# Optimization experiments

Hardware: AMD Instinct MI355X
Metric: run time of the kernel (lower is better)

## Reference

```python
import jax, jax.numpy as jnp
import numpy as np

N_NODES = 50000
N_EDGES = 640000
D = 128  # node_dim == edge_dim (required by gate * Vh[dst])
BN_EPS = 1e-5


def _bn(x, gamma, beta):
    # BatchNorm1d in training mode: batch stats over dim 0, biased variance.
    mu = jnp.mean(x, axis=0)
    var = jnp.var(x, axis=0)
    return (x - mu) * jax.lax.rsqrt(var + BN_EPS) * gamma + beta


def setup_inputs() -> dict:
    key = jax.random.key(0)
    ks = jax.random.split(key, 12)
    s = 1.0 / np.sqrt(D)
    h = jax.random.normal(ks[0], (N_NODES, D), dtype=jnp.float32)
    e = jax.random.normal(ks[1], (N_EDGES, D), dtype=jnp.float32)
    edge_index = jax.random.randint(ks[2], (2, N_EDGES), 0, N_NODES)
    mk = lambda k: jax.random.uniform(k, (D, D), jnp.float32, -s, s)
    return {
        "h": h, "e": e, "edge_index": edge_index,
        "Pw": mk(ks[3]), "Qw": mk(ks[4]), "Rw": mk(ks[5]),
        "Uw": mk(ks[6]), "Vw": mk(ks[7]),
        "W1": mk(ks[8]), "b1": jnp.zeros((D,), jnp.float32),
        "W2": mk(ks[9]), "b2": jnp.zeros((D,), jnp.float32),
        "gamma_e": jnp.ones((D,), jnp.float32), "beta_e": jnp.zeros((D,), jnp.float32),
        "gamma_n": jnp.ones((D,), jnp.float32), "beta_n": jnp.zeros((D,), jnp.float32),
        "alpha": jnp.float32(1.0),
    }


def reference(h, e, edge_index, Pw, Qw, Rw, Uw, Vw, W1, b1, W2, b2,
              gamma_e, beta_e, gamma_n, beta_n, alpha):
    src, dst = edge_index[0], edge_index[1]
    # e_hat = P e + Q h[src] + R h[dst]   -> [E, D]
    e_hat = e @ Pw + h[src] @ Qw + h[dst] @ Rw
    # edge update: residual + MLP(BN(e_hat))
    z = _bn(e_hat, gamma_e, beta_e)
    e_new = e + jax.nn.relu(z @ W1 + b1) @ W2 + b2
    # node update: h + alpha * BN(U h + sum_j sigmoid(e_hat) * V h[dst])
    gate = jax.nn.sigmoid(e_hat)
    Vh = h @ Vw
    msg = gate * Vh[dst]                         # [E, D]
    agg = jax.ops.segment_sum(msg, src, num_segments=h.shape[0])
    h_new = h + alpha * _bn(h @ Uw + agg, gamma_n, beta_n)
    return (h_new, e_new)
```

## Files before the change

kernel.cpp:

```cpp
#include <hip/hip_runtime.h>


#define NN 50000
#define NE 640000
#define D 128

typedef unsigned int uint32;
typedef unsigned short u16;
typedef short bf16x8 __attribute__((ext_vector_type(8)));
typedef float floatx4 __attribute__((ext_vector_type(4)));

__device__ __forceinline__ u16 f2bf(float f) {
  uint32 u = __float_as_uint(f);
  u += 0x7fffu + ((u >> 16) & 1u);
  return (u16)(u >> 16);
}
__device__ __forceinline__ float bfu2f(uint32 lo16) { return __uint_as_float(lo16 << 16); }
__device__ __forceinline__ uint32 pack2(float a, float b) {
  return (uint32)f2bf(a) | ((uint32)f2bf(b) << 16);
}

__device__ __forceinline__ void mfma_tile64(const u16* __restrict__ Xs,
                                            const u16* __restrict__ Ws,
                                            floatx4 acc[8], int wave, int lane) {
  const int q = lane >> 4, l = lane & 15;
  const u16* ax = Xs + (wave * 16 + l) * 136 + q * 8;
  const u16* bx = Ws + l * 136 + q * 8;
#pragma unroll
  for (int kk = 0; kk < 4; ++kk) {
    bf16x8 a = *(const bf16x8*)(ax + kk * 32);
#pragma unroll
    for (int nt = 0; nt < 8; ++nt) {
      bf16x8 b = *(const bf16x8*)(bx + nt * 16 * 136 + kk * 32);
      acc[nt] = __builtin_amdgcn_mfma_f32_16x16x32_bf16(a, b, acc[nt], 0, 0, 0);
    }
  }
}

__global__ __launch_bounds__(256) void k_wconv(
    const float* __restrict__ Pw, const float* __restrict__ Qw, const float* __restrict__ Rw,
    const float* __restrict__ Uw, const float* __restrict__ Vw, const float* __restrict__ W1,
    const float* __restrict__ W2, u16* __restrict__ wt) {
  int b = blockIdx.x;
  const float* s = (b == 0) ? Pw : (b == 1) ? Qw : (b == 2) ? Rw : (b == 3) ? Uw
                 : (b == 4) ? Vw : (b == 5) ? W1 : W2;
  u16* dstp = wt + b * 16384;
  for (int idx = threadIdx.x; idx < 16384; idx += 256) {
    int k = idx >> 7, n = idx & 127;
    dstp[n * 128 + k] = f2bf(s[idx]);
  }
}

__global__ __launch_bounds__(256) void k_node_gemm(
    const float* __restrict__ h, const u16* __restrict__ wt, float* __restrict__ hQ,
    float* __restrict__ hR, float* __restrict__ hU, float* __restrict__ hV) {
  __shared__ u16 Xs[64 * 136];
  __shared__ u16 Ws[128 * 136];
  const int tid = threadIdx.x;
  const int wave = tid >> 6, lane = tid & 63;
  const int q = lane >> 4, l = lane & 15;
  const int row0 = blockIdx.x * 64;

#pragma unroll
  for (int it = 0; it < 8; ++it) {
    int idx = (it * 256 + tid) * 4;
    int r = idx >> 7, c = idx & 127;
    int g = row0 + r;
    float4 v = make_float4(0.f, 0.f, 0.f, 0.f);
    if (g < NN) v = *(const float4*)(h + (size_t)g * D + c);
    uint2 p;
    p.x = pack2(v.x, v.y);
    p.y = pack2(v.z, v.w);
    *(uint2*)(Xs + r * 136 + c) = p;
  }

  float* const outs[4] = {hQ, hR, hU, hV};
#pragma unroll
  for (int wi = 0; wi < 4; ++wi) {
#pragma unroll
    for (int it = 0; it < 8; ++it) {
      int idx = (it * 256 + tid) * 8;
      *(uint4*)(Ws + (idx >> 7) * 136 + (idx & 127)) =
          *(const uint4*)(wt + (wi + 1) * 16384 + idx);
    }
    __syncthreads();
    floatx4 acc[8] = {};
    mfma_tile64(Xs, Ws, acc, wave, lane);
    float* outp = outs[wi];
#pragma unroll
    for (int nt = 0; nt < 8; ++nt) {
#pragma unroll
      for (int r = 0; r < 4; ++r) {
        int m = wave * 16 + q * 4 + r;
        int g = row0 + m;
        if (g < NN) outp[(size_t)g * D + nt * 16 + l] = acc[nt][r];
      }
    }
    __syncthreads();
  }
}

__global__ __launch_bounds__(256) void k_hist(const int* __restrict__ src,
                                              int* __restrict__ cnt) {
  int i = blockIdx.x * 256 + threadIdx.x;
  if (i < NE) atomicAdd(&cnt[src[i]], 1);
}

__global__ __launch_bounds__(1024) void k_scan(const int* __restrict__ cnt,
                                               int* __restrict__ offs) {
  __shared__ int part[1024];
  const int t = threadIdx.x;
  const int base = t * 49;
  int s = 0;
  for (int j = 0; j < 49; ++j) {
    int i = base + j;
    if (i < NN) s += cnt[i];
  }
  part[t] = s;
  __syncthreads();
  for (int d = 1; d < 1024; d <<= 1) {
    int v = (t >= d) ? part[t - d] : 0;
    __syncthreads();
    part[t] += v;
    __syncthreads();
  }
  int run = (t == 0) ? 0 : part[t - 1];
  for (int j = 0; j < 49; ++j) {
    int i = base + j;
    if (i < NN) {
      offs[i] = run;
      run += cnt[i];
    }
  }
}

__global__ __launch_bounds__(256) void k_scatter(const int* __restrict__ src,
                                                 const int* __restrict__ dst,
                                                 int* __restrict__ offs,
                                                 int2* __restrict__ sorted) {
  int i = blockIdx.x * 256 + threadIdx.x;
  if (i < NE) {
    int s = src[i];
    int p = atomicAdd(&offs[s], 1);
    sorted[p] = make_int2(i, dst[i]);
  }
}

__global__ __launch_bounds__(256) void k_edge1(
    const float* __restrict__ e, const int* __restrict__ src, const int* __restrict__ dst,
    const u16* __restrict__ wt, const float* __restrict__ hQ, const float* __restrict__ hR,
    u16* __restrict__ ehat, float* __restrict__ esum, float* __restrict__ esq) {
  __shared__ u16 Xs[64 * 136];
  __shared__ u16 Ws[128 * 136];
  __shared__ int sSrc[64], sDst[64];
  __shared__ float sSum[128], sSq[128];
  const int tid = threadIdx.x;
  const int wave = tid >> 6, lane = tid & 63;
  const int q = lane >> 4, l = lane & 15;
  const int row0 = blockIdx.x * 64;

  if (tid < 128) { sSum[tid] = 0.f; sSq[tid] = 0.f; }
  if (tid < 64) { sSrc[tid] = src[row0 + tid]; sDst[tid] = dst[row0 + tid]; }
#pragma unroll
  for (int it = 0; it < 8; ++it) {
    int idx = (it * 256 + tid) * 4;
    int r = idx >> 7, c = idx & 127;
    float4 v = *(const float4*)(e + (size_t)(row0 + r) * D + c);
    uint2 p;
    p.x = pack2(v.x, v.y);
    p.y = pack2(v.z, v.w);
    *(uint2*)(Xs + r * 136 + c) = p;
  }
#pragma unroll
  for (int it = 0; it < 8; ++it) {
    int idx = (it * 256 + tid) * 8;
    *(uint4*)(Ws + (idx >> 7) * 136 + (idx & 127)) = *(const uint4*)(wt + idx);
  }
  __syncthreads();

  floatx4 acc[8] = {};
  mfma_tile64(Xs, Ws, acc, wave, lane);

  float cs[8] = {}, cq[8] = {};
#pragma unroll
  for (int nt = 0; nt < 8; ++nt) {
    const int n = nt * 16 + l;
#pragma unroll
    for (int r = 0; r < 4; ++r) {
      const int m = wave * 16 + q * 4 + r;
      const int s = sSrc[m], dd = sDst[m];
      float v = acc[nt][r] + hQ[(size_t)s * D + n] + hR[(size_t)dd * D + n];
      ehat[(size_t)(row0 + m) * D + n] = f2bf(v);
      cs[nt] += v;
      cq[nt] += v * v;
    }
  }
#pragma unroll
  for (int nt = 0; nt < 8; ++nt) {
    cs[nt] += __shfl_xor(cs[nt], 16);
    cs[nt] += __shfl_xor(cs[nt], 32);
    cq[nt] += __shfl_xor(cq[nt], 16);
    cq[nt] += __shfl_xor(cq[nt], 32);
    if (q == 0) {
      atomicAdd(&sSum[nt * 16 + l], cs[nt]);
      atomicAdd(&sSq[nt * 16 + l], cq[nt]);
    }
  }
  __syncthreads();
  if (tid < 128) {
    atomicAdd(&esum[(blockIdx.x & 31) * D + tid], sSum[tid]);
    atomicAdd(&esq[(blockIdx.x & 31) * D + tid], sSq[tid]);
  }
}

__global__ __launch_bounds__(256) void k_agg(
    const u16* __restrict__ ehat, const float* __restrict__ hV, const float* __restrict__ hU,
    const int* __restrict__ cnt, const int* __restrict__ offs, const int2* __restrict__ sorted,
    float* __restrict__ xb, float* __restrict__ nsum, float* __restrict__ nsq) {
  __shared__ float sSum[128], sSq[128];
  const int tid = threadIdx.x;
  if (tid < 128) { sSum[tid] = 0.f; sSq[tid] = 0.f; }
  __syncthreads();
  const int lane = tid & 31;
  const int n = blockIdx.x * 8 + (tid >> 5);
  const int end = offs[n];
  const int deg = cnt[n];
  const int p0 = end - deg;
  float4 acc = make_float4(0.f, 0.f, 0.f, 0.f);
  for (int k = 0; k < deg; ++k) {
    int2 ed = sorted[p0 + k];
    uint2 ev = *(const uint2*)(ehat + (size_t)ed.x * D + lane * 4);
    float4 v = *(const float4*)(hV + (size_t)ed.y * D + lane * 4);
    acc.x += v.x / (1.f + __expf(-bfu2f(ev.x & 0xffffu)));
    acc.y += v.y / (1.f + __expf(-bfu2f(ev.x >> 16)));
    acc.z += v.z / (1.f + __expf(-bfu2f(ev.y & 0xffffu)));
    acc.w += v.w / (1.f + __expf(-bfu2f(ev.y >> 16)));
  }
  float4 u = *(const float4*)(hU + (size_t)n * D + lane * 4);
  float4 x = make_float4(u.x + acc.x, u.y + acc.y, u.z + acc.z, u.w + acc.w);
  *(float4*)(xb + (size_t)n * D + lane * 4) = x;
  atomicAdd(&sSum[lane * 4 + 0], x.x);
  atomicAdd(&sSum[lane * 4 + 1], x.y);
  atomicAdd(&sSum[lane * 4 + 2], x.z);
  atomicAdd(&sSum[lane * 4 + 3], x.w);
  atomicAdd(&sSq[lane * 4 + 0], x.x * x.x);
  atomicAdd(&sSq[lane * 4 + 1], x.y * x.y);
  atomicAdd(&sSq[lane * 4 + 2], x.z * x.z);
  atomicAdd(&sSq[lane * 4 + 3], x.w * x.w);
  __syncthreads();
  if (tid < 128) {
    atomicAdd(&nsum[(blockIdx.x & 31) * D + tid], sSum[tid]);
    atomicAdd(&nsq[(blockIdx.x & 31) * D + tid], sSq[tid]);
  }
}

__global__ __launch_bounds__(128) void k_finalize(
    const float* __restrict__ esum, const float* __restrict__ esq,
    const float* __restrict__ nsum, const float* __restrict__ nsq,
    const float* __restrict__ ge, const float* __restrict__ be, const float* __restrict__ gn,
    const float* __restrict__ bnb, float* __restrict__ sce, float* __restrict__ she,
    float* __restrict__ scn, float* __restrict__ shn) {
  const int t = threadIdx.x;
  float s = 0.f, q = 0.f;
  for (int i = 0; i < 32; ++i) { s += esum[i * D + t]; q += esq[i * D + t]; }
  float mean = s / (float)NE;
  float var = q / (float)NE - mean * mean;
  float istd = rsqrtf(var + 1e-5f);
  sce[t] = istd * ge[t];
  she[t] = be[t] - mean * istd * ge[t];
  s = 0.f; q = 0.f;
  for (int i = 0; i < 32; ++i) { s += nsum[i * D + t]; q += nsq[i * D + t]; }
  mean = s / (float)NN;
  var = q / (float)NN - mean * mean;
  istd = rsqrtf(var + 1e-5f);
  scn[t] = istd * gn[t];
  shn[t] = bnb[t] - mean * istd * gn[t];
}

__global__ __launch_bounds__(256) void k_edge2(
    const u16* __restrict__ ehat, const float* __restrict__ e, const u16* __restrict__ wt,
    const float* __restrict__ sce, const float* __restrict__ she, const float* __restrict__ b1,
    const float* __restrict__ b2, float* __restrict__ oute) {
  __shared__ u16 Ts[64 * 136];
  __shared__ u16 Ws[128 * 136];
  __shared__ float sSc[128], sSh[128], sB1[128], sB2[128];
  const int tid = threadIdx.x;
  const int wave = tid >> 6, lane = tid & 63;
  const int q = lane >> 4, l = lane & 15;
  const int row0 = blockIdx.x * 64;

  if (tid < 128) { sSc[tid] = sce[tid]; sSh[tid] = she[tid]; sB1[tid] = b1[tid]; sB2[tid] = b2[tid]; }
  __syncthreads();

#pragma unroll
  for (int it = 0; it < 4; ++it) {
    int idx = (it * 256 + tid) * 8;
    int r = idx >> 7, c = idx & 127;
    uint4 u = *(const uint4*)(ehat + (size_t)(row0 + r) * D + c);
    float f0 = bfu2f(u.x & 0xffffu) * sSc[c + 0] + sSh[c + 0];
    float f1 = bfu2f(u.x >> 16) * sSc[c + 1] + sSh[c + 1];
    float f2 = bfu2f(u.y & 0xffffu) * sSc[c + 2] + sSh[c + 2];
    float f3 = bfu2f(u.y >> 16) * sSc[c + 3] + sSh[c + 3];
    float f4 = bfu2f(u.z & 0xffffu) * sSc[c + 4] + sSh[c + 4];
    float f5 = bfu2f(u.z >> 16) * sSc[c + 5] + sSh[c + 5];
    float f6 = bfu2f(u.w & 0xffffu) * sSc[c + 6] + sSh[c + 6];
    float f7 = bfu2f(u.w >> 16) * sSc[c + 7] + sSh[c + 7];
    uint4 o;
    o.x = pack2(f0, f1); o.y = pack2(f2, f3); o.z = pack2(f4, f5); o.w = pack2(f6, f7);
    *(uint4*)(Ts + r * 136 + c) = o;
  }
#pragma unroll
  for (int it = 0; it < 8; ++it) {
    int idx = (it * 256 + tid) * 8;
    *(uint4*)(Ws + (idx >> 7) * 136 + (idx & 127)) = *(const uint4*)(wt + 5 * 16384 + idx);
  }
  __syncthreads();

  floatx4 acc[8] = {};
  mfma_tile64(Ts, Ws, acc, wave, lane);
  __syncthreads();

#pragma unroll
  for (int nt = 0; nt < 8; ++nt) {
    int n = nt * 16 + l;
#pragma unroll
    for (int r = 0; r < 4; ++r) {
      int m = wave * 16 + q * 4 + r;
      float v = acc[nt][r] + sB1[n];
      Ts[m * 136 + n] = f2bf(fmaxf(v, 0.f));
    }
  }
#pragma unroll
  for (int it = 0; it < 8; ++it) {
    int idx = (it * 256 + tid) * 8;
    *(uint4*)(Ws + (idx >> 7) * 136 + (idx & 127)) = *(const uint4*)(wt + 6 * 16384 + idx);
  }
  __syncthreads();

  floatx4 acc2[8] = {};
  mfma_tile64(Ts, Ws, acc2, wave, lane);

#pragma unroll
  for (int nt = 0; nt < 8; ++nt) {
    int n = nt * 16 + l;
#pragma unroll
    for (int r = 0; r < 4; ++r) {
      int m = wave * 16 + q * 4 + r;
      size_t gi = (size_t)(row0 + m) * D + n;
      oute[gi] = e[gi] + acc2[nt][r] + sB2[n];
    }
  }
}

__global__ __launch_bounds__(256) void k_node_out(
    const float* __restrict__ h, const float* __restrict__ xb,
    const float* __restrict__ scn, const float* __restrict__ shn,
    const float* __restrict__ alphap, float* __restrict__ outh) {
  size_t idx = ((size_t)blockIdx.x * 256 + threadIdx.x) * 4;
  int c = (int)(idx & 127);
  float al = alphap[0];
  float4 x = *(const float4*)(xb + idx);
  float4 hh = *(const float4*)(h + idx);
  float4 o;
  o.x = hh.x + al * (x.x * scn[c + 0] + shn[c + 0]);
  o.y = hh.y + al * (x.y * scn[c + 1] + shn[c + 1]);
  o.z = hh.z + al * (x.z * scn[c + 2] + shn[c + 2]);
  o.w = hh.w + al * (x.w * scn[c + 3] + shn[c + 3]);
  *(float4*)(outh + idx) = o;
}

extern "C" void kernel_launch(void* const* d_in, const int* in_sizes, int n_in, void* d_out,
                              int out_size, void* d_ws, size_t ws_size, hipStream_t stream) {
  const float* h = (const float*)d_in[0];
  const float* e = (const float*)d_in[1];
  const int* ei = (const int*)d_in[2];
  const float* Pw = (const float*)d_in[3];
  const float* Qw = (const float*)d_in[4];
  const float* Rw = (const float*)d_in[5];
  const float* Uw = (const float*)d_in[6];
  const float* Vw = (const float*)d_in[7];
  const float* W1 = (const float*)d_in[8];
  const float* b1 = (const float*)d_in[9];
  const float* W2 = (const float*)d_in[10];
  const float* b2 = (const float*)d_in[11];
  const float* ge = (const float*)d_in[12];
  const float* be = (const float*)d_in[13];
  const float* gn = (const float*)d_in[14];
  const float* bnb = (const float*)d_in[15];
  const float* al = (const float*)d_in[16];

  const int* srcp = ei;
  const int* dstp = ei + NE;

  char* ws = (char*)d_ws;
  u16* wt = (u16*)(ws);
  float* hQ = (float*)(ws + 229376ull);
  float* hR = (float*)(ws + 229376ull + 1ull * 25600000ull);
  float* hU = (float*)(ws + 229376ull + 2ull * 25600000ull);
  float* hV = (float*)(ws + 229376ull + 3ull * 25600000ull);
  float* xb = (float*)(ws + 229376ull + 4ull * 25600000ull);
  u16* ehat = (u16*)(ws + 229376ull + 5ull * 25600000ull);
  char* statb = ws + 229376ull + 5ull * 25600000ull + 163840000ull;
  float* esum = (float*)(statb);
  float* esq = (float*)(statb + 16384);
  float* nsum = (float*)(statb + 32768);
  float* nsq = (float*)(statb + 49152);
  float* sce = (float*)(statb + 65536);
  float* she = (float*)(statb + 65536 + 512);
  float* scn = (float*)(statb + 65536 + 1024);
  float* shn = (float*)(statb + 65536 + 1536);
  char* sortb = statb + 67584;
  int* cnt = (int*)(sortb);
  int* offs = (int*)(sortb + 200704);
  int2* sorted = (int2*)(sortb + 401408);

  float* outh = (float*)d_out;
  float* oute = outh + (size_t)NN * D;

  hipMemsetAsync(cnt, 0, 200704, stream);
  hipMemsetAsync(statb, 0, 65536, stream);

  k_wconv<<<7, 256, 0, stream>>>(Pw, Qw, Rw, Uw, Vw, W1, W2, wt);
  k_hist<<<2500, 256, 0, stream>>>(srcp, cnt);
  k_scan<<<1, 1024, 0, stream>>>(cnt, offs);
  k_scatter<<<2500, 256, 0, stream>>>(srcp, dstp, offs, sorted);
  k_node_gemm<<<782, 256, 0, stream>>>(h, wt, hQ, hR, hU, hV);
  k_edge1<<<10000, 256, 0, stream>>>(e, srcp, dstp, wt, hQ, hR, ehat, esum, esq);
  k_agg<<<6250, 256, 0, stream>>>(ehat, hV, hU, cnt, offs, sorted, xb, nsum, nsq);
  k_finalize<<<1, 128, 0, stream>>>(esum, esq, nsum, nsq, ge, be, gn, bnb, sce, she, scn, shn);
  k_edge2<<<10000, 256, 0, stream>>>(ehat, e, wt, sce, she, b1, b2, oute);
  k_node_out<<<6250, 256, 0, stream>>>(h, xb, scn, shn, al, outh);
}
```

Before: 1.204 ms.

## Halve weight LDS tiles, unroll edge aggregation gathers, merge memsets

The GEMM kernels now stage the 128x128 weight matrix in two 64-row halves with extra barriers. This halves the Ws shared buffer and adds launch_bounds min-blocks hints so more blocks can be resident per CU. The k_agg loop is unrolled by four to issue independent gathers of ehat and hV, and sigmoid now uses a hardware reciprocal instead of a division. The two memsets are merged into one. In exchange the GEMMs gain barriers and a second weight-staging pass, and the launch bounds may force register limits.

Measured after the change: 1.137 ms. 5.6% less time.

```diff
diff --git a/kernel.cpp b/kernel.cpp
--- a/kernel.cpp
+++ b/kernel.cpp
@@ -19,10 +19,13 @@
 __device__ __forceinline__ uint32 pack2(float a, float b) {
   return (uint32)f2bf(a) | ((uint32)f2bf(b) << 16);
 }
-
-__device__ __forceinline__ void mfma_tile64(const u16* __restrict__ Xs,
-                                            const u16* __restrict__ Ws,
-                                            floatx4 acc[8], int wave, int lane) {
+__device__ __forceinline__ float fsigmoid(float x) {
+  return __builtin_amdgcn_rcpf(1.f + __expf(-x));
+}
+
+__device__ __forceinline__ void mfma_half(const u16* __restrict__ Xs,
+                                          const u16* __restrict__ Ws,
+                                          floatx4* __restrict__ acc, int wave, int lane) {
   const int q = lane >> 4, l = lane & 15;
   const u16* ax = Xs + (wave * 16 + l) * 136 + q * 8;
   const u16* bx = Ws + l * 136 + q * 8;
@@ -30,10 +33,19 @@
   for (int kk = 0; kk < 4; ++kk) {
     bf16x8 a = *(const bf16x8*)(ax + kk * 32);
 #pragma unroll
-    for (int nt = 0; nt < 8; ++nt) {
+    for (int nt = 0; nt < 4; ++nt) {
       bf16x8 b = *(const bf16x8*)(bx + nt * 16 * 136 + kk * 32);
       acc[nt] = __builtin_amdgcn_mfma_f32_16x16x32_bf16(a, b, acc[nt], 0, 0, 0);
     }
+  }
+}
+
+__device__ __forceinline__ void stage_whalf(u16* __restrict__ Ws, const u16* __restrict__ wsrc,
+                                            int tid) {
+#pragma unroll
+  for (int it = 0; it < 4; ++it) {
+    int idx = (it * 256 + tid) * 8;
+    *(uint4*)(Ws + (idx >> 7) * 136 + (idx & 127)) = *(const uint4*)(wsrc + idx);
   }
 }
 
@@ -51,11 +63,11 @@
   }
 }
 
-__global__ __launch_bounds__(256) void k_node_gemm(
+__global__ __launch_bounds__(256, 4) void k_node_gemm(
     const float* __restrict__ h, const u16* __restrict__ wt, float* __restrict__ hQ,
     float* __restrict__ hR, float* __restrict__ hU, float* __restrict__ hV) {
   __shared__ u16 Xs[64 * 136];
-  __shared__ u16 Ws[128 * 136];
+  __shared__ u16 Ws[64 * 136];
   const int tid = threadIdx.x;
   const int wave = tid >> 6, lane = tid & 63;
   const int q = lane >> 4, l = lane & 15;
@@ -77,15 +89,15 @@
   float* const outs[4] = {hQ, hR, hU, hV};
 #pragma unroll
   for (int wi = 0; wi < 4; ++wi) {
-#pragma unroll
-    for (int it = 0; it < 8; ++it) {
-      int idx = (it * 256 + tid) * 8;
-      *(uint4*)(Ws + (idx >> 7) * 136 + (idx & 127)) =
-          *(const uint4*)(wt + (wi + 1) * 16384 + idx);
-    }
+    __syncthreads();
+    stage_whalf(Ws, wt + (wi + 1) * 16384, tid);
     __syncthreads();
     floatx4 acc[8] = {};
-    mfma_tile64(Xs, Ws, acc, wave, lane);
+    mfma_half(Xs, Ws, acc, wave, lane);
+    __syncthreads();
+    stage_whalf(Ws, wt + (wi + 1) * 16384 + 8192, tid);
+    __syncthreads();
+    mfma_half(Xs, Ws, acc + 4, wave, lane);
     float* outp = outs[wi];
 #pragma unroll
     for (int nt = 0; nt < 8; ++nt) {
@@ -96,7 +108,6 @@
         if (g < NN) outp[(size_t)g * D + nt * 16 + l] = acc[nt][r];
       }
     }
-    __syncthreads();
   }
 }
 
@@ -112,6 +123,7 @@
   const int t = threadIdx.x;
   const int base = t * 49;
   int s = 0;
+#pragma unroll 7
   for (int j = 0; j < 49; ++j) {
     int i = base + j;
     if (i < NN) s += cnt[i];
@@ -146,12 +158,12 @@
   }
 }
 
-__global__ __launch_bounds__(256) void k_edge1(
+__global__ __launch_bounds__(256, 4) void k_edge1(
     const float* __restrict__ e, const int* __restrict__ src, const int* __restrict__ dst,
     const u16* __restrict__ wt, const float* __restrict__ hQ, const float* __restrict__ hR,
     u16* __restrict__ ehat, float* __restrict__ esum, float* __restrict__ esq) {
   __shared__ u16 Xs[64 * 136];
-  __shared__ u16 Ws[128 * 136];
+  __shared__ u16 Ws[64 * 136];
   __shared__ int sSrc[64], sDst[64];
   __shared__ float sSum[128], sSq[128];
   const int tid = threadIdx.x;
@@ -171,15 +183,15 @@
     p.y = pack2(v.z, v.w);
     *(uint2*)(Xs + r * 136 + c) = p;
   }
-#pragma unroll
-  for (int it = 0; it < 8; ++it) {
-    int idx = (it * 256 + tid) * 8;
-    *(uint4*)(Ws + (idx >> 7) * 136 + (idx & 127)) = *(const uint4*)(wt + idx);
-  }
+  stage_whalf(Ws, wt, tid);
   __syncthreads();
 
   floatx4 acc[8] = {};
-  mfma_tile64(Xs, Ws, acc, wave, lane);
+  mfma_half(Xs, Ws, acc, wave, lane);
+  __syncthreads();
+  stage_whalf(Ws, wt + 8192, tid);
+  __syncthreads();
+  mfma_half(Xs, Ws, acc + 4, wave, lane);
 
   float cs[8] = {}, cq[8] = {};
 #pragma unroll
@@ -226,27 +238,59 @@
   const int end = offs[n];
   const int deg = cnt[n];
   const int p0 = end - deg;
+  const int c4 = lane * 4;
   float4 acc = make_float4(0.f, 0.f, 0.f, 0.f);
-  for (int k = 0; k < deg; ++k) {
+  int k = 0;
+  for (; k + 4 <= deg; k += 4) {
+    int2 ed0 = sorted[p0 + k + 0];
+    int2 ed1 = sorted[p0 + k + 1];
+    int2 ed2 = sorted[p0 + k + 2];
+    int2 ed3 = sorted[p0 + k + 3];
+    uint2 ev0 = *(const uint2*)(ehat + (size_t)ed0.x * D + c4);
+    uint2 ev1 = *(const uint2*)(ehat + (size_t)ed1.x * D + c4);
+    uint2 ev2 = *(const uint2*)(ehat + (size_t)ed2.x * D + c4);
+    uint2 ev3 = *(const uint2*)(ehat + (size_t)ed3.x * D + c4);
+    float4 v0 = *(const float4*)(hV + (size_t)ed0.y * D + c4);
+    float4 v1 = *(const float4*)(hV + (size_t)ed1.y * D + c4);
+    float4 v2 = *(const float4*)(hV + (size_t)ed2.y * D + c4);
+    float4 v3 = *(const float4*)(hV + (size_t)ed3.y * D + c4);
+    acc.x += v0.x * fsigmoid(bfu2f(ev0.x & 0xffffu));
+    acc.y += v0.y * fsigmoid(bfu2f(ev0.x >> 16));
+    acc.z += v0.z * fsigmoid(bfu2f(ev0.y & 0xffffu));
+    acc.w += v0.w * fsigmoid(bfu2f(ev0.y >> 16));
+    acc.x += v1.x * fsigmoid(bfu2f(ev1.x & 0xffffu));
+    acc.y += v1.y * fsigmoid(bfu2f(ev1.x >> 16));
+    acc.z += v1.z * fsigmoid(bfu2f(ev1.y & 0xffffu));
+    acc.w += v1.w * fsigmoid(bfu2f(ev1.y >> 16));
+    acc.x += v2.x * fsigmoid(bfu2f(ev2.x & 0xffffu));
+    acc.y += v2.y * fsigmoid(bfu2f(ev2.x >> 16));
+    acc.z += v2.z * fsigmoid(bfu2f(ev2.y & 0xffffu));
+    acc.w += v2.w * fsigmoid(bfu2f(ev2.y >> 16));
+    acc.x += v3.x * fsigmoid(bfu2f(ev3.x & 0xffffu));
+    acc.y += v3.y * fsigmoid(bfu2f(ev3.x >> 16));
+    acc.z += v3.z * fsigmoid(bfu2f(ev3.y & 0xffffu));
+    acc.w += v3.w * fsigmoid(bfu2f(ev3.y >> 16));
+  }
+  for (; k < deg; ++k) {
     int2 ed = sorted[p0 + k];
-    uint2 ev = *(const uint2*)(ehat + (size_t)ed.x * D + lane * 4);
-    float4 v = *(const float4*)(hV + (size_t)ed.y * D + lane * 4);
-    acc.x += v.x / (1.f + __expf(-bfu2f(ev.x & 0xffffu)));
-    acc.y += v.y / (1.f + __expf(-bfu2f(ev.x >> 16)));
-    acc.z += v.z / (1.f + __expf(-bfu2f(ev.y & 0xffffu)));
-    acc.w += v.w / (1.f + __expf(-bfu2f(ev.y >> 16)));
-  }
-  float4 u = *(const float4*)(hU + (size_t)n * D + lane * 4);
+    uint2 ev = *(const uint2*)(ehat + (size_t)ed.x * D + c4);
+    float4 v = *(const float4*)(hV + (size_t)ed.y * D + c4);
+    acc.x += v.x * fsigmoid(bfu2f(ev.x & 0xffffu));
+    acc.y += v.y * fsigmoid(bfu2f(ev.x >> 16));
+    acc.z += v.z * fsigmoid(bfu2f(ev.y & 0xffffu));
+    acc.w += v.w * fsigmoid(bfu2f(ev.y >> 16));
+  }
+  float4 u = *(const float4*)(hU + (size_t)n * D + c4);
   float4 x = make_float4(u.x + acc.x, u.y + acc.y, u.z + acc.z, u.w + acc.w);
-  *(float4*)(xb + (size_t)n * D + lane * 4) = x;
-  atomicAdd(&sSum[lane * 4 + 0], x.x);
-  atomicAdd(&sSum[lane * 4 + 1], x.y);
-  atomicAdd(&sSum[lane * 4 + 2], x.z);
-  atomicAdd(&sSum[lane * 4 + 3], x.w);
-  atomicAdd(&sSq[lane * 4 + 0], x.x * x.x);
-  atomicAdd(&sSq[lane * 4 + 1], x.y * x.y);
-  atomicAdd(&sSq[lane * 4 + 2], x.z * x.z);
-  atomicAdd(&sSq[lane * 4 + 3], x.w * x.w);
+  *(float4*)(xb + (size_t)n * D + c4) = x;
+  atomicAdd(&sSum[c4 + 0], x.x);
+  atomicAdd(&sSum[c4 + 1], x.y);
+  atomicAdd(&sSum[c4 + 2], x.z);
+  atomicAdd(&sSum[c4 + 3], x.w);
+  atomicAdd(&sSq[c4 + 0], x.x * x.x);
+  atomicAdd(&sSq[c4 + 1], x.y * x.y);
+  atomicAdd(&sSq[c4 + 2], x.z * x.z);
+  atomicAdd(&sSq[c4 + 3], x.w * x.w);
   __syncthreads();
   if (tid < 128) {
     atomicAdd(&nsum[(blockIdx.x & 31) * D + tid], sSum[tid]);
@@ -277,12 +321,12 @@
   shn[t] = bnb[t] - mean * istd * gn[t];
 }
 
-__global__ __launch_bounds__(256) void k_edge2(
+__global__ __launch_bounds__(256, 4) void k_edge2(
     const u16* __restrict__ ehat, const float* __restrict__ e, const u16* __restrict__ wt,
     const float* __restrict__ sce, const float* __restrict__ she, const float* __restrict__ b1,
     const float* __restrict__ b2, float* __restrict__ oute) {
   __shared__ u16 Ts[64 * 136];
-  __shared__ u16 Ws[128 * 136];
+  __shared__ u16 Ws[64 * 136];
   __shared__ float sSc[128], sSh[128], sB1[128], sB2[128];
   const int tid = threadIdx.x;
   const int wave = tid >> 6, lane = tid & 63;
@@ -309,15 +353,15 @@
     o.x = pack2(f0, f1); o.y = pack2(f2, f3); o.z = pack2(f4, f5); o.w = pack2(f6, f7);
     *(uint4*)(Ts + r * 136 + c) = o;
   }
-#pragma unroll
-  for (int it = 0; it < 8; ++it) {
-    int idx = (it * 256 + tid) * 8;
-    *(uint4*)(Ws + (idx >> 7) * 136 + (idx & 127)) = *(const uint4*)(wt + 5 * 16384 + idx);
-  }
+  stage_whalf(Ws, wt + 5 * 16384, tid);
   __syncthreads();
 
   floatx4 acc[8] = {};
-  mfma_tile64(Ts, Ws, acc, wave, lane);
+  mfma_half(Ts, Ws, acc, wave, lane);
+  __syncthreads();
+  stage_whalf(Ws, wt + 5 * 16384 + 8192, tid);
+  __syncthreads();
+  mfma_half(Ts, Ws, acc + 4, wave, lane);
   __syncthreads();
 
 #pragma unroll
@@ -330,15 +374,15 @@
       Ts[m * 136 + n] = f2bf(fmaxf(v, 0.f));
     }
   }
-#pragma unroll
-  for (int it = 0; it < 8; ++it) {
-    int idx = (it * 256 + tid) * 8;
-    *(uint4*)(Ws + (idx >> 7) * 136 + (idx & 127)) = *(const uint4*)(wt + 6 * 16384 + idx);
-  }
+  stage_whalf(Ws, wt + 6 * 16384, tid);
   __syncthreads();
 
   floatx4 acc2[8] = {};
-  mfma_tile64(Ts, Ws, acc2, wave, lane);
+  mfma_half(Ts, Ws, acc2, wave, lane);
+  __syncthreads();
+  stage_whalf(Ws, wt + 6 * 16384 + 8192, tid);
+  __syncthreads();
+  mfma_half(Ts, Ws, acc2 + 4, wave, lane);
 
 #pragma unroll
   for (int nt = 0; nt < 8; ++nt) {
@@ -417,8 +461,7 @@
   float* outh = (float*)d_out;
   float* oute = outh + (size_t)NN * D;
 
-  hipMemsetAsync(cnt, 0, 200704, stream);
-  hipMemsetAsync(statb, 0, 65536, stream);
+  hipMemsetAsync(statb, 0, 67584 + 200704, stream);
 
   k_wconv<<<7, 256, 0, stream>>>(Pw, Qw, Rw, Uw, Vw, W1, W2, wt);
   k_hist<<<2500, 256, 0, stream>>>(srcp, cnt);
```
